# Optimization experiments

Hardware: AMD Instinct MI355X
Metric: run time of the kernel (lower is better)

The kernel has to match this reference:

```python
import jax, jax.numpy as jnp
import numpy as np

HIDDEN = 2048
NUM_HEADS = 32
NUM_GROUPS = 8
HEAD_DIM = HIDDEN // NUM_HEADS          # 64
GROUP_DIM = HEAD_DIM * NUM_GROUPS       # 512
HPG = NUM_HEADS // NUM_GROUPS           # heads per group = 4
B, S = 2, 2048


def setup_inputs() -> dict:
    key = jax.random.key(0)
    ks = jax.random.split(key, 6)
    sd = 1.0 / np.sqrt(HIDDEN)
    return {
        "x": jax.random.normal(ks[0], (B, S, HIDDEN), jnp.float32),
        "mask": jnp.ones((1, 1, S, S), jnp.int32),
        "Wq": jax.random.normal(ks[1], (HIDDEN, HIDDEN), jnp.float32) * sd,
        "bq": jnp.zeros((HIDDEN,), jnp.float32),
        "Wk": jax.random.normal(ks[2], (HIDDEN, GROUP_DIM), jnp.float32) * sd,
        "bk": jnp.zeros((GROUP_DIM,), jnp.float32),
        "Wv": jax.random.normal(ks[3], (HIDDEN, GROUP_DIM), jnp.float32) * sd,
        "bv": jnp.zeros((GROUP_DIM,), jnp.float32),
        "Wo": jax.random.normal(ks[4], (HIDDEN, HIDDEN), jnp.float32) * sd,
        "bo": jnp.zeros((HIDDEN,), jnp.float32),
    }


def reference(x, mask, Wq, bq, Wk, bk, Wv, bv, Wo, bo):
    b, s, _ = x.shape
    # projections
    q = x @ Wq + bq                                        # [B,S,H*d]
    k = x @ Wk + bk                                        # [B,S,G*d]
    v = x @ Wv + bv
    # split heads: q heads are group-major (g, p) to match the torch view
    q = q.reshape(b, s, NUM_GROUPS, HPG, HEAD_DIM)         # [B,S,G,P,d]
    k = k.reshape(b, s, NUM_GROUPS, HEAD_DIM)              # [B,S,G,d]
    v = v.reshape(b, s, NUM_GROUPS, HEAD_DIM)
    scale = 1.0 / np.sqrt(HEAD_DIM).astype(np.float32)
    # grouped attention without materializing repeated K/V
    scores = jnp.einsum('bsgpd,btgd->bgpst', q, k) * scale  # [B,G,P,S,T]
    if mask is not None:
        m = mask[:, :, None]                                # [1,1,1,S,T]
        scores = jnp.where(m == 0, jnp.float32(-1e9), scores)
    weights = jax.nn.softmax(scores, axis=-1)
    out = jnp.einsum('bgpst,btgd->bsgpd', weights, v)       # [B,S,G,P,d]
    out = out.reshape(b, s, HIDDEN)
    return out @ Wo + bo
```

## Files before the change

kernel.cpp:

```cpp
#include <hip/hip_runtime.h>
#include <hip/hip_bf16.h>


#define DEVINL __device__ __forceinline__

typedef __attribute__((ext_vector_type(8))) short bf16x8;
typedef __attribute__((ext_vector_type(4))) float f32x4;

DEVINL unsigned short f2bf(float f) {
  unsigned u = __builtin_bit_cast(unsigned, f);
  u += 0x7fffu + ((u >> 16) & 1u);
  return (unsigned short)(u >> 16);
}

DEVINL unsigned pk2bf(float a, float b) {
  __hip_bfloat162 h = __float22bfloat162_rn(float2{a, b});
  unsigned r;
  __builtin_memcpy(&r, &h, 4);
  return r;
}

DEVINL void gl_lds16(const void* g, void* l) {
  __builtin_amdgcn_global_load_lds(
      (const __attribute__((address_space(1))) void*)g,
      (__attribute__((address_space(3))) void*)l, 16, 0, 0);
}

__global__ __launch_bounds__(256)
void prep_k(const float* __restrict__ x,
            const float* __restrict__ Wq, const float* __restrict__ Wk,
            const float* __restrict__ Wv, const float* __restrict__ Wo,
            const int* __restrict__ mask,
            unsigned short* __restrict__ xb,
            unsigned short* __restrict__ WqT, unsigned short* __restrict__ WkT,
            unsigned short* __restrict__ WvT, unsigned short* __restrict__ WoT,
            int* __restrict__ flags)
{
  __shared__ float tile[64][68];
  __shared__ int fl[4];
  int blk = blockIdx.x;
  const int tid = threadIdx.x;
  if (blk < 4096) {
    size_t base = (size_t)blk * 2048 + tid * 8;
    float4 f0 = *(const float4*)&x[base];
    float4 f1 = *(const float4*)&x[base + 4];
    uint4 o;
    o.x = pk2bf(f0.x, f0.y); o.y = pk2bf(f0.z, f0.w);
    o.z = pk2bf(f1.x, f1.y); o.w = pk2bf(f1.z, f1.w);
    *(uint4*)&xb[base] = o;
    return;
  }
  blk -= 4096;
  if (blk >= 2560) {
    int fb = blk - 2560;
    int qt = fb >> 5, tt = fb & 31;
    bool hz = false;
#pragma unroll
    for (int it = 0; it < 8; ++it) {
      int l = it * 1024 + tid * 4;
      int row = l >> 6, col = l & 63;
      int4 mv = *(const int4*)&mask[(size_t)(qt * 128 + row) * 2048 + tt * 64 + col];
      hz |= (mv.x == 0) | (mv.y == 0) | (mv.z == 0) | (mv.w == 0);
    }
    unsigned long long bal = __ballot(hz);
    if ((tid & 63) == 0) fl[tid >> 6] = (bal != 0ull) ? 1 : 0;
    __syncthreads();
    if (tid == 0) flags[fb] = fl[0] | fl[1] | fl[2] | fl[3];
    return;
  }
  const float* W; unsigned short* WT; int N;
  if (blk < 1024)      { W = Wq; WT = WqT; N = 2048; }
  else if (blk < 1280) { W = Wk; WT = WkT; N = 512;  blk -= 1024; }
  else if (blk < 1536) { W = Wv; WT = WvT; N = 512;  blk -= 1280; }
  else                 { W = Wo; WT = WoT; N = 2048; blk -= 1536; }
  const int kt = blk & 31, nt = blk >> 5;
  const int k0 = kt * 64, n0 = nt * 64;
  const int tr = tid >> 4, tc4 = (tid & 15) * 4;
#pragma unroll
  for (int it = 0; it < 4; ++it) {
    int k = it * 16 + tr;
    float4 v = *(const float4*)&W[(size_t)(k0 + k) * N + n0 + tc4];
    tile[tc4 + 0][k] = v.x; tile[tc4 + 1][k] = v.y;
    tile[tc4 + 2][k] = v.z; tile[tc4 + 3][k] = v.w;
  }
  __syncthreads();
#pragma unroll
  for (int it = 0; it < 4; ++it) {
    int n = it * 16 + tr;
    uint2 o;
    o.x = pk2bf(tile[n][tc4 + 0], tile[n][tc4 + 1]);
    o.y = pk2bf(tile[n][tc4 + 2], tile[n][tc4 + 3]);
    *(uint2*)&WT[(size_t)(n0 + n) * 2048 + k0 + tc4] = o;
  }
}

__global__ __launch_bounds__(256)
void mm_qkv(const unsigned short* __restrict__ A,
            const unsigned short* __restrict__ Wt,
            const float* __restrict__ bq, const float* __restrict__ bk,
            const float* __restrict__ bv,
            unsigned short* __restrict__ qb, unsigned short* __restrict__ kb,
            unsigned short* __restrict__ vb)
{
  __shared__ __align__(16) unsigned short As[128 * 32];
  __shared__ __align__(16) unsigned short Bs[128 * 32];
  const int tid = threadIdx.x;
  const int lane = tid & 63, w = tid >> 6;
  const int l15 = lane & 15, quad = lane >> 4;
  const int wm = w & 1, wn = w >> 1;
  const int row0 = blockIdx.y * 128;
  const int col0 = blockIdx.x * 128;

  f32x4 acc[4][4];
#pragma unroll
  for (int mt = 0; mt < 4; ++mt)
#pragma unroll
    for (int nt = 0; nt < 4; ++nt) acc[mt][nt] = (f32x4){0.f, 0.f, 0.f, 0.f};

  const int c0 = tid, c1 = 256 + tid;
  const size_t aoff0 = (size_t)(row0 + (c0 >> 2)) * 2048 + (c0 & 3) * 8;
  const size_t aoff1 = (size_t)(row0 + (c1 >> 2)) * 2048 + (c1 & 3) * 8;
  const size_t boff0 = (size_t)(col0 + (c0 >> 2)) * 2048 + (c0 & 3) * 8;
  const size_t boff1 = (size_t)(col0 + (c1 >> 2)) * 2048 + (c1 & 3) * 8;

  for (int k0 = 0; k0 < 2048; k0 += 32) {
    gl_lds16(A + aoff0 + k0, As + (size_t)c0 * 8);
    gl_lds16(A + aoff1 + k0, As + (size_t)c1 * 8);
    gl_lds16(Wt + boff0 + k0, Bs + (size_t)c0 * 8);
    gl_lds16(Wt + boff1 + k0, Bs + (size_t)c1 * 8);
    __syncthreads();
    bf16x8 af[4], bfr[4];
#pragma unroll
    for (int mt = 0; mt < 4; ++mt)
      af[mt] = *(const bf16x8*)&As[(wm * 64 + mt * 16 + l15) * 32 + quad * 8];
#pragma unroll
    for (int nt = 0; nt < 4; ++nt)
      bfr[nt] = *(const bf16x8*)&Bs[(wn * 64 + nt * 16 + l15) * 32 + quad * 8];
#pragma unroll
    for (int mt = 0; mt < 4; ++mt)
#pragma unroll
      for (int nt = 0; nt < 4; ++nt)
        acc[mt][nt] = __builtin_amdgcn_mfma_f32_16x16x32_bf16(
            af[mt], bfr[nt], acc[mt][nt], 0, 0, 0);
    __syncthreads();
  }

  const int rbase = row0 + wm * 64 + quad * 4;
#pragma unroll
  for (int nt = 0; nt < 4; ++nt) {
    const int cg = col0 + wn * 64 + nt * 16 + l15;
#pragma unroll
    for (int mt = 0; mt < 4; ++mt) {
#pragma unroll
      for (int reg = 0; reg < 4; ++reg) {
        const int r = rbase + mt * 16 + reg;
        const int bb = r >> 11, ss = r & 2047;
        float v = acc[mt][nt][reg];
        if (col0 < 2048) {
          v += bq[cg];
          int g = cg >> 8, p = (cg >> 6) & 3, d = cg & 63;
          qb[(((size_t)((bb * 8 + g) * 4 + p)) * 2048 + ss) * 64 + d] =
              f2bf(v * 0.1803368801111244f);
        } else if (col0 < 2560) {
          int cl = cg - 2048;
          v += bk[cl];
          int g = cl >> 6, d = cl & 63;
          kb[((size_t)(bb * 8 + g) * 2048 + ss) * 64 + d] = f2bf(v);
        } else {
          int cl = cg - 2560;
          v += bv[cl];
          int g = cl >> 6, d = cl & 63;
          vb[((size_t)(bb * 8 + g) * 64 + d) * 2048 + ss] = f2bf(v);
        }
      }
    }
  }
}

__global__ __launch_bounds__(256)
void mm_out(const unsigned short* __restrict__ A,
            const unsigned short* __restrict__ Bt,
            const float* __restrict__ bias, float* __restrict__ Of)
{
  __shared__ __align__(16) unsigned short As[128 * 32];
  __shared__ __align__(16) unsigned short Bs[128 * 32];
  const int tid = threadIdx.x;
  const int lane = tid & 63, w = tid >> 6;
  const int l15 = lane & 15, quad = lane >> 4;
  const int wm = w & 1, wn = w >> 1;
  const int row0 = blockIdx.y * 128;
  const int col0 = blockIdx.x * 128;

  f32x4 acc[4][4];
#pragma unroll
  for (int mt = 0; mt < 4; ++mt)
#pragma unroll
    for (int nt = 0; nt < 4; ++nt) acc[mt][nt] = (f32x4){0.f, 0.f, 0.f, 0.f};

  const int c0 = tid, c1 = 256 + tid;
  const size_t aoff0 = (size_t)(row0 + (c0 >> 2)) * 2048 + (c0 & 3) * 8;
  const size_t aoff1 = (size_t)(row0 + (c1 >> 2)) * 2048 + (c1 & 3) * 8;
  const size_t boff0 = (size_t)(col0 + (c0 >> 2)) * 2048 + (c0 & 3) * 8;
  const size_t boff1 = (size_t)(col0 + (c1 >> 2)) * 2048 + (c1 & 3) * 8;

  for (int k0 = 0; k0 < 2048; k0 += 32) {
    gl_lds16(A + aoff0 + k0, As + (size_t)c0 * 8);
    gl_lds16(A + aoff1 + k0, As + (size_t)c1 * 8);
    gl_lds16(Bt + boff0 + k0, Bs + (size_t)c0 * 8);
    gl_lds16(Bt + boff1 + k0, Bs + (size_t)c1 * 8);
    __syncthreads();
    bf16x8 af[4], bfr[4];
#pragma unroll
    for (int mt = 0; mt < 4; ++mt)
      af[mt] = *(const bf16x8*)&As[(wm * 64 + mt * 16 + l15) * 32 + quad * 8];
#pragma unroll
    for (int nt = 0; nt < 4; ++nt)
      bfr[nt] = *(const bf16x8*)&Bs[(wn * 64 + nt * 16 + l15) * 32 + quad * 8];
#pragma unroll
    for (int mt = 0; mt < 4; ++mt)
#pragma unroll
      for (int nt = 0; nt < 4; ++nt)
        acc[mt][nt] = __builtin_amdgcn_mfma_f32_16x16x32_bf16(
            af[mt], bfr[nt], acc[mt][nt], 0, 0, 0);
    __syncthreads();
  }

  const int rbase = row0 + wm * 64 + quad * 4;
#pragma unroll
  for (int nt = 0; nt < 4; ++nt) {
    const int cg = col0 + wn * 64 + nt * 16 + l15;
    const float bvv = bias[cg];
#pragma unroll
    for (int mt = 0; mt < 4; ++mt)
#pragma unroll
      for (int reg = 0; reg < 4; ++reg) {
        const int r = rbase + mt * 16 + reg;
        Of[(size_t)r * 2048 + cg] = acc[mt][nt][reg] + bvv;
      }
  }
}

__global__ __launch_bounds__(256, 3)
void attn_k(const unsigned short* __restrict__ qb,
            const unsigned short* __restrict__ kb,
            const unsigned short* __restrict__ vb,
            const int* __restrict__ mask, const int* __restrict__ flags,
            unsigned short* __restrict__ attnb)
{
  __shared__ __align__(16) unsigned short Ks[2][64 * 64];
  __shared__ __align__(16) unsigned short Vs[2][64 * 64];
  __shared__ __align__(16) unsigned short Ps[128 * 72];
  const int tid = threadIdx.x;
  const int lane = tid & 63, w = tid >> 6;
  const int l15 = lane & 15, quad = lane >> 4;
  const int q0 = blockIdx.x * 128;
  const int pr = blockIdx.y;
  const int b = pr >> 5, g = (pr >> 2) & 7, p = pr & 3;
  const int bg = b * 8 + g;

  const unsigned short* Kg = kb + (size_t)bg * 2048 * 64;
  const unsigned short* Vg = vb + (size_t)bg * 64 * 2048;
  const unsigned short* Qg = qb + (size_t)(bg * 4 + p) * 2048 * 64;

  bf16x8 qf[2][2];
#pragma unroll
  for (int u = 0; u < 2; ++u) {
    const size_t qrow = (size_t)(q0 + w * 32 + u * 16 + l15) * 64;
    qf[u][0] = *(const bf16x8*)&Qg[qrow + quad * 8];
    qf[u][1] = *(const bf16x8*)&Qg[qrow + 32 + quad * 8];
  }

  bf16x8 ones;
#pragma unroll
  for (int i = 0; i < 8; ++i) ones[i] = (short)0x3F80;

  f32x4 acc_o[4][2];
  f32x4 acc_l[2];
#pragma unroll
  for (int u = 0; u < 2; ++u) acc_l[u] = (f32x4){0.f, 0.f, 0.f, 0.f};
#pragma unroll
  for (int dt = 0; dt < 4; ++dt)
#pragma unroll
    for (int u = 0; u < 2; ++u) acc_o[dt][u] = (f32x4){0.f, 0.f, 0.f, 0.f};

  const int c0 = tid, c1 = 256 + tid;
  const int kr0 = c0 >> 3, kx0 = ((c0 & 7) ^ (kr0 & 7)) * 8;
  const int kr1 = c1 >> 3, kx1 = ((c1 & 7) ^ (kr1 & 7)) * 8;

  gl_lds16(Kg + (size_t)kr0 * 64 + kx0, &Ks[0][(size_t)c0 * 8]);
  gl_lds16(Kg + (size_t)kr1 * 64 + kx1, &Ks[0][(size_t)c1 * 8]);
  gl_lds16(Vg + (size_t)kr0 * 2048 + kx0, &Vs[0][(size_t)c0 * 8]);
  gl_lds16(Vg + (size_t)kr1 * 2048 + kx1, &Vs[0][(size_t)c1 * 8]);
  __syncthreads();

  for (int it = 0; it < 32; ++it) {
    const int cur = it & 1;
    const int t0 = it << 6;
    if (it < 31) {
      const int tn = t0 + 64;
      gl_lds16(Kg + (size_t)(tn + kr0) * 64 + kx0, &Ks[cur ^ 1][(size_t)c0 * 8]);
      gl_lds16(Kg + (size_t)(tn + kr1) * 64 + kx1, &Ks[cur ^ 1][(size_t)c1 * 8]);
      gl_lds16(Vg + (size_t)kr0 * 2048 + tn + kx0, &Vs[cur ^ 1][(size_t)c0 * 8]);
      gl_lds16(Vg + (size_t)kr1 * 2048 + tn + kx1, &Vs[cur ^ 1][(size_t)c1 * 8]);
    }
    const unsigned short* Kc = Ks[cur];
    const unsigned short* Vc = Vs[cur];

    bf16x8 kf[4][2];
#pragma unroll
    for (int nt = 0; nt < 4; ++nt) {
      const int trow = nt * 16 + l15, ks = trow & 7;
      kf[nt][0] = *(const bf16x8*)&Kc[trow * 64 + ((quad ^ ks) * 8)];
      kf[nt][1] = *(const bf16x8*)&Kc[trow * 64 + (((4 + quad) ^ ks) * 8)];
    }
    const bool msk = flags[blockIdx.x * 32 + it] != 0;

#pragma unroll
    for (int u = 0; u < 2; ++u) {
      f32x4 st[4];
#pragma unroll
      for (int nt = 0; nt < 4; ++nt) {
        f32x4 z = (f32x4){0.f, 0.f, 0.f, 0.f};
        z = __builtin_amdgcn_mfma_f32_16x16x32_bf16(kf[nt][0], qf[u][0], z, 0, 0, 0);
        st[nt] = __builtin_amdgcn_mfma_f32_16x16x32_bf16(kf[nt][1], qf[u][1], z, 0, 0, 0);
      }
      if (msk) {
        const size_t mrow = (size_t)(q0 + w * 32 + u * 16 + l15) * 2048;
#pragma unroll
        for (int nt = 0; nt < 4; ++nt) {
          int4 mv = *(const int4*)&mask[mrow + t0 + nt * 16 + quad * 4];
          if (mv.x == 0) st[nt][0] = -1e30f;
          if (mv.y == 0) st[nt][1] = -1e30f;
          if (mv.z == 0) st[nt][2] = -1e30f;
          if (mv.w == 0) st[nt][3] = -1e30f;
        }
      }
      const int srow = w * 32 + u * 16 + l15;
#pragma unroll
      for (int nt = 0; nt < 4; ++nt) {
        float p0 = __builtin_amdgcn_exp2f(st[nt][0]);
        float p1 = __builtin_amdgcn_exp2f(st[nt][1]);
        float p2 = __builtin_amdgcn_exp2f(st[nt][2]);
        float p3 = __builtin_amdgcn_exp2f(st[nt][3]);
        uint2 pkd;
        pkd.x = pk2bf(p0, p1);
        pkd.y = pk2bf(p2, p3);
        *(uint2*)&Ps[srow * 72 + nt * 16 + quad * 4] = pkd;
      }
    }
    asm volatile("s_waitcnt lgkmcnt(0)" ::: "memory");

    bf16x8 pf[2][2];
#pragma unroll
    for (int u = 0; u < 2; ++u) {
      const int srow = w * 32 + u * 16 + l15;
      pf[u][0] = *(const bf16x8*)&Ps[srow * 72 + quad * 8];
      pf[u][1] = *(const bf16x8*)&Ps[srow * 72 + 32 + quad * 8];
      acc_l[u] = __builtin_amdgcn_mfma_f32_16x16x32_bf16(ones, pf[u][0], acc_l[u], 0, 0, 0);
      acc_l[u] = __builtin_amdgcn_mfma_f32_16x16x32_bf16(ones, pf[u][1], acc_l[u], 0, 0, 0);
    }
#pragma unroll
    for (int dt = 0; dt < 4; ++dt) {
      const int drow = dt * 16 + l15, ks = drow & 7;
      bf16x8 v0 = *(const bf16x8*)&Vc[drow * 64 + ((quad ^ ks) * 8)];
      bf16x8 v1 = *(const bf16x8*)&Vc[drow * 64 + (((4 + quad) ^ ks) * 8)];
#pragma unroll
      for (int u = 0; u < 2; ++u) {
        acc_o[dt][u] = __builtin_amdgcn_mfma_f32_16x16x32_bf16(v0, pf[u][0], acc_o[dt][u], 0, 0, 0);
        acc_o[dt][u] = __builtin_amdgcn_mfma_f32_16x16x32_bf16(v1, pf[u][1], acc_o[dt][u], 0, 0, 0);
      }
    }
    __syncthreads();
  }

  const int hh = g * 4 + p;
#pragma unroll
  for (int u = 0; u < 2; ++u) {
    const float inv = 1.0f / acc_l[u][0];
    const int s = q0 + w * 32 + u * 16 + l15;
#pragma unroll
    for (int dt = 0; dt < 4; ++dt) {
      uint2 o;
      o.x = pk2bf(acc_o[dt][u][0] * inv, acc_o[dt][u][1] * inv);
      o.y = pk2bf(acc_o[dt][u][2] * inv, acc_o[dt][u][3] * inv);
      *(uint2*)&attnb[((size_t)(b * 2048 + s)) * 2048 + hh * 64 + dt * 16 + quad * 4] = o;
    }
  }
}

extern "C" void kernel_launch(void* const* d_in, const int* in_sizes, int n_in,
                              void* d_out, int out_size, void* d_ws, size_t ws_size,
                              hipStream_t stream)
{
  (void)in_sizes; (void)n_in; (void)out_size; (void)ws_size;
  const float* x  = (const float*)d_in[0];
  const int* mask = (const int*)d_in[1];
  const float* Wq = (const float*)d_in[2];
  const float* bq = (const float*)d_in[3];
  const float* Wk = (const float*)d_in[4];
  const float* bk = (const float*)d_in[5];
  const float* Wv = (const float*)d_in[6];
  const float* bv = (const float*)d_in[7];
  const float* Wo = (const float*)d_in[8];
  const float* bo = (const float*)d_in[9];
  float* out = (float*)d_out;

  unsigned short* xb  = (unsigned short*)d_ws;
  unsigned short* WqT = xb  + 8388608;
  unsigned short* WkT = WqT + 4194304;
  unsigned short* WvT = WkT + 1048576;
  unsigned short* WoT = WvT + 1048576;
  unsigned short* qb  = WoT + 4194304;
  unsigned short* kb  = qb  + 8388608;
  unsigned short* vb  = kb  + 2097152;
  int* flags = (int*)(vb + 2097152);
  unsigned short* attnb = xb;

  dim3 blk(256);
  hipLaunchKernelGGL(prep_k, dim3(7168), blk, 0, stream,
                     x, Wq, Wk, Wv, Wo, mask, xb, WqT, WkT, WvT, WoT, flags);
  hipLaunchKernelGGL(mm_qkv, dim3(24, 32), blk, 0, stream,
                     xb, WqT, bq, bk, bv, qb, kb, vb);
  hipLaunchKernelGGL(attn_k, dim3(16, 64), blk, 0, stream,
                     qb, kb, vb, mask, flags, attnb);
  hipLaunchKernelGGL(mm_out, dim3(16, 32), blk, 0, stream,
                     attnb, WoT, bo, out);
}
```

Before: 348.8 us.

## Rework projection GEMMs into 256x256-tile, multi-stage pipelined, swizzled LDS kernels

Both projection GEMMs (QKV and output) now share a macro-based main loop. Each 512-thread block computes a 256x256 tile and streams K in 32-wide halves with global_load_lds. Loads are kept in flight across stages with vmcnt waits and raw barriers instead of a full sync per step, and the LDS layout uses an XOR swizzle to avoid bank conflicts. MFMA sections are wrapped in s_setprio to favour math issue. The larger tiles cut global traffic and synchronisation, but they shrink the grids to 192 and 128 blocks, which may leave many CUs idle, and they use about 128KB of LDS per block.

```diff
diff --git a/kernel.cpp b/kernel.cpp
--- a/kernel.cpp
+++ b/kernel.cpp
@@ -94,7 +94,85 @@
   }
 }
 
-__global__ __launch_bounds__(256)
+
+#define GEMM_WAITB() do { \
+    asm volatile("s_waitcnt vmcnt(8)" ::: "memory"); \
+    __builtin_amdgcn_s_barrier(); \
+  } while (0)
+
+#define GEMM_STAGE(t, kh) do { \
+    const int _b = (t) & 1; \
+    const size_t _ko = (size_t)(t) * 64 + (kh) * 32; \
+    unsigned short* _lA = As + ((_b * 2 + (kh)) * 8192) + tid * 8; \
+    unsigned short* _lB = Bs + ((_b * 2 + (kh)) * 8192) + tid * 8; \
+    gl_lds16(Asrc0 + _ko, _lA); \
+    gl_lds16(Asrc1 + _ko, _lA + 4096); \
+    gl_lds16(Bsrc0 + _ko, _lB); \
+    gl_lds16(Bsrc1 + _ko, _lB + 4096); \
+  } while (0)
+
+#define GEMM_HALFGROUP(t, kh) do { \
+    bf16x8 bfr[4]; \
+    const unsigned short* _base = As + (((t) & 1) * 2 + (kh)) * 8192; \
+    const unsigned short* _bbase = Bs + (((t) & 1) * 2 + (kh)) * 8192; \
+    _Pragma("unroll") \
+    for (int nt = 0; nt < 4; ++nt) { \
+      const int brow = wn * 64 + nt * 16 + l15; \
+      bfr[nt] = *(const bf16x8*)&_bbase[brow * 32 + ((quad ^ ((brow >> 1) & 3)) * 8)]; \
+    } \
+    _Pragma("unroll") \
+    for (int mh = 0; mh < 2; ++mh) { \
+      bf16x8 af[4]; \
+      _Pragma("unroll") \
+      for (int mt = 0; mt < 4; ++mt) { \
+        const int arow = wm * 128 + mh * 64 + mt * 16 + l15; \
+        af[mt] = *(const bf16x8*)&_base[arow * 32 + ((quad ^ ((arow >> 1) & 3)) * 8)]; \
+      } \
+      __builtin_amdgcn_s_setprio(1); \
+      _Pragma("unroll") \
+      for (int mt = 0; mt < 4; ++mt) \
+        _Pragma("unroll") \
+        for (int nt = 0; nt < 4; ++nt) \
+          acc[mh * 4 + mt][nt] = __builtin_amdgcn_mfma_f32_16x16x32_bf16( \
+              af[mt], bfr[nt], acc[mh * 4 + mt][nt], 0, 0, 0); \
+      __builtin_amdgcn_s_setprio(0); \
+    } \
+  } while (0)
+
+#define GEMM_KLOOP_BODY(Aptr, Bptr) \
+  const int tid = threadIdx.x; \
+  const int lane = tid & 63, l15 = lane & 15, quad = lane >> 4; \
+  const int w = tid >> 6, wm = w & 1, wn = w >> 1; \
+  const int row0 = blockIdx.y * 256; \
+  const int col0 = blockIdx.x * 256; \
+  f32x4 acc[8][4]; \
+  _Pragma("unroll") \
+  for (int am = 0; am < 8; ++am) \
+    _Pragma("unroll") \
+    for (int nt = 0; nt < 4; ++nt) acc[am][nt] = (f32x4){0.f, 0.f, 0.f, 0.f}; \
+  const int e0 = tid, e1 = tid + 512; \
+  const int sr0 = e0 >> 2, sc0 = ((e0 & 3) ^ ((sr0 >> 1) & 3)) * 8; \
+  const int sr1 = e1 >> 2, sc1 = ((e1 & 3) ^ ((sr1 >> 1) & 3)) * 8; \
+  const unsigned short* Asrc0 = (Aptr) + (size_t)(row0 + sr0) * 2048 + sc0; \
+  const unsigned short* Asrc1 = (Aptr) + (size_t)(row0 + sr1) * 2048 + sc1; \
+  const unsigned short* Bsrc0 = (Bptr) + (size_t)(col0 + sr0) * 2048 + sc0; \
+  const unsigned short* Bsrc1 = (Bptr) + (size_t)(col0 + sr1) * 2048 + sc1; \
+  GEMM_STAGE(0, 0); \
+  GEMM_STAGE(0, 1); \
+  GEMM_STAGE(1, 0); \
+  GEMM_WAITB(); \
+  for (int t = 0; t < 32; ++t) { \
+    const int tn1 = (t + 1 < 32) ? t + 1 : 31; \
+    const int tn2 = (t + 2 < 32) ? t + 2 : 31; \
+    GEMM_STAGE(tn1, 1); \
+    GEMM_HALFGROUP(t, 0); \
+    GEMM_WAITB(); \
+    GEMM_STAGE(tn2, 0); \
+    GEMM_HALFGROUP(t, 1); \
+    GEMM_WAITB(); \
+  }
+
+__global__ __launch_bounds__(512, 2)
 void mm_qkv(const unsigned short* __restrict__ A,
             const unsigned short* __restrict__ Wt,
             const float* __restrict__ bq, const float* __restrict__ bk,
@@ -102,60 +180,21 @@
             unsigned short* __restrict__ qb, unsigned short* __restrict__ kb,
             unsigned short* __restrict__ vb)
 {
-  __shared__ __align__(16) unsigned short As[128 * 32];
-  __shared__ __align__(16) unsigned short Bs[128 * 32];
-  const int tid = threadIdx.x;
-  const int lane = tid & 63, w = tid >> 6;
-  const int l15 = lane & 15, quad = lane >> 4;
-  const int wm = w & 1, wn = w >> 1;
-  const int row0 = blockIdx.y * 128;
-  const int col0 = blockIdx.x * 128;
-
-  f32x4 acc[4][4];
-#pragma unroll
-  for (int mt = 0; mt < 4; ++mt)
-#pragma unroll
-    for (int nt = 0; nt < 4; ++nt) acc[mt][nt] = (f32x4){0.f, 0.f, 0.f, 0.f};
-
-  const int c0 = tid, c1 = 256 + tid;
-  const size_t aoff0 = (size_t)(row0 + (c0 >> 2)) * 2048 + (c0 & 3) * 8;
-  const size_t aoff1 = (size_t)(row0 + (c1 >> 2)) * 2048 + (c1 & 3) * 8;
-  const size_t boff0 = (size_t)(col0 + (c0 >> 2)) * 2048 + (c0 & 3) * 8;
-  const size_t boff1 = (size_t)(col0 + (c1 >> 2)) * 2048 + (c1 & 3) * 8;
-
-  for (int k0 = 0; k0 < 2048; k0 += 32) {
-    gl_lds16(A + aoff0 + k0, As + (size_t)c0 * 8);
-    gl_lds16(A + aoff1 + k0, As + (size_t)c1 * 8);
-    gl_lds16(Wt + boff0 + k0, Bs + (size_t)c0 * 8);
-    gl_lds16(Wt + boff1 + k0, Bs + (size_t)c1 * 8);
-    __syncthreads();
-    bf16x8 af[4], bfr[4];
-#pragma unroll
-    for (int mt = 0; mt < 4; ++mt)
-      af[mt] = *(const bf16x8*)&As[(wm * 64 + mt * 16 + l15) * 32 + quad * 8];
-#pragma unroll
-    for (int nt = 0; nt < 4; ++nt)
-      bfr[nt] = *(const bf16x8*)&Bs[(wn * 64 + nt * 16 + l15) * 32 + quad * 8];
-#pragma unroll
-    for (int mt = 0; mt < 4; ++mt)
-#pragma unroll
-      for (int nt = 0; nt < 4; ++nt)
-        acc[mt][nt] = __builtin_amdgcn_mfma_f32_16x16x32_bf16(
-            af[mt], bfr[nt], acc[mt][nt], 0, 0, 0);
-    __syncthreads();
-  }
-
-  const int rbase = row0 + wm * 64 + quad * 4;
+  __shared__ __align__(16) unsigned short As[32768];
+  __shared__ __align__(16) unsigned short Bs[32768];
+  GEMM_KLOOP_BODY(A, Wt)
+
+  const int rb = row0 + wm * 128 + quad * 4;
 #pragma unroll
   for (int nt = 0; nt < 4; ++nt) {
     const int cg = col0 + wn * 64 + nt * 16 + l15;
 #pragma unroll
-    for (int mt = 0; mt < 4; ++mt) {
+    for (int am = 0; am < 8; ++am) {
 #pragma unroll
       for (int reg = 0; reg < 4; ++reg) {
-        const int r = rbase + mt * 16 + reg;
+        const int r = rb + am * 16 + reg;
         const int bb = r >> 11, ss = r & 2047;
-        float v = acc[mt][nt][reg];
+        float v = acc[am][nt][reg];
         if (col0 < 2048) {
           v += bq[cg];
           int g = cg >> 8, p = (cg >> 6) & 3, d = cg & 63;
@@ -177,66 +216,28 @@
   }
 }
 
-__global__ __launch_bounds__(256)
+__global__ __launch_bounds__(512, 2)
 void mm_out(const unsigned short* __restrict__ A,
             const unsigned short* __restrict__ Bt,
             const float* __restrict__ bias, float* __restrict__ Of)
 {
-  __shared__ __align__(16) unsigned short As[128 * 32];
-  __shared__ __align__(16) unsigned short Bs[128 * 32];
-  const int tid = threadIdx.x;
-  const int lane = tid & 63, w = tid >> 6;
-  const int l15 = lane & 15, quad = lane >> 4;
-  const int wm = w & 1, wn = w >> 1;
-  const int row0 = blockIdx.y * 128;
-  const int col0 = blockIdx.x * 128;
-
-  f32x4 acc[4][4];
-#pragma unroll
-  for (int mt = 0; mt < 4; ++mt)
-#pragma unroll
-    for (int nt = 0; nt < 4; ++nt) acc[mt][nt] = (f32x4){0.f, 0.f, 0.f, 0.f};
-
-  const int c0 = tid, c1 = 256 + tid;
-  const size_t aoff0 = (size_t)(row0 + (c0 >> 2)) * 2048 + (c0 & 3) * 8;
-  const size_t aoff1 = (size_t)(row0 + (c1 >> 2)) * 2048 + (c1 & 3) * 8;
-  const size_t boff0 = (size_t)(col0 + (c0 >> 2)) * 2048 + (c0 & 3) * 8;
-  const size_t boff1 = (size_t)(col0 + (c1 >> 2)) * 2048 + (c1 & 3) * 8;
-
-  for (int k0 = 0; k0 < 2048; k0 += 32) {
-    gl_lds16(A + aoff0 + k0, As + (size_t)c0 * 8);
-    gl_lds16(A + aoff1 + k0, As + (size_t)c1 * 8);
-    gl_lds16(Bt + boff0 + k0, Bs + (size_t)c0 * 8);
-    gl_lds16(Bt + boff1 + k0, Bs + (size_t)c1 * 8);
-    __syncthreads();
-    bf16x8 af[4], bfr[4];
-#pragma unroll
-    for (int mt = 0; mt < 4; ++mt)
-      af[mt] = *(const bf16x8*)&As[(wm * 64 + mt * 16 + l15) * 32 + quad * 8];
-#pragma unroll
-    for (int nt = 0; nt < 4; ++nt)
-      bfr[nt] = *(const bf16x8*)&Bs[(wn * 64 + nt * 16 + l15) * 32 + quad * 8];
-#pragma unroll
-    for (int mt = 0; mt < 4; ++mt)
-#pragma unroll
-      for (int nt = 0; nt < 4; ++nt)
-        acc[mt][nt] = __builtin_amdgcn_mfma_f32_16x16x32_bf16(
-            af[mt], bfr[nt], acc[mt][nt], 0, 0, 0);
-    __syncthreads();
-  }
-
-  const int rbase = row0 + wm * 64 + quad * 4;
+  __shared__ __align__(16) unsigned short As[32768];
+  __shared__ __align__(16) unsigned short Bs[32768];
+  GEMM_KLOOP_BODY(A, Bt)
+
+  const int rb = row0 + wm * 128 + quad * 4;
 #pragma unroll
   for (int nt = 0; nt < 4; ++nt) {
     const int cg = col0 + wn * 64 + nt * 16 + l15;
     const float bvv = bias[cg];
 #pragma unroll
-    for (int mt = 0; mt < 4; ++mt)
+    for (int am = 0; am < 8; ++am) {
 #pragma unroll
       for (int reg = 0; reg < 4; ++reg) {
-        const int r = rbase + mt * 16 + reg;
-        Of[(size_t)r * 2048 + cg] = acc[mt][nt][reg] + bvv;
-      }
+        const int r = rb + am * 16 + reg;
+        Of[(size_t)r * 2048 + cg] = acc[am][nt][reg] + bvv;
+      }
+    }
   }
 }
 
@@ -416,13 +417,12 @@
   int* flags = (int*)(vb + 2097152);
   unsigned short* attnb = xb;
 
-  dim3 blk(256);
-  hipLaunchKernelGGL(prep_k, dim3(7168), blk, 0, stream,
+  hipLaunchKernelGGL(prep_k, dim3(7168), dim3(256), 0, stream,
                      x, Wq, Wk, Wv, Wo, mask, xb, WqT, WkT, WvT, WoT, flags);
-  hipLaunchKernelGGL(mm_qkv, dim3(24, 32), blk, 0, stream,
+  hipLaunchKernelGGL(mm_qkv, dim3(12, 16), dim3(512), 0, stream,
                      xb, WqT, bq, bk, bv, qb, kb, vb);
-  hipLaunchKernelGGL(attn_k, dim3(16, 64), blk, 0, stream,
+  hipLaunchKernelGGL(attn_k, dim3(16, 64), dim3(256), 0, stream,
                      qb, kb, vb, mask, flags, attnb);
-  hipLaunchKernelGGL(mm_out, dim3(16, 32), blk, 0, stream,
+  hipLaunchKernelGGL(mm_out, dim3(8, 16), dim3(512), 0, stream,
                      attnb, WoT, bo, out);
 }
```

Measured after the change: 383.6 us. 10.0% more time.

## Double attention block to 512 threads and 256 query rows, remap block order

Applied to the files above, without the earlier changes.

The attention kernel now runs 8 waves per block covering 256 query rows, so each K/V tile staged in LDS is shared by twice as many waves, and each thread issues one async global-to-LDS load per K and V tile instead of two. Blocks are remapped so that consecutive block ids fall on different (batch, group, head) pairs. The mask-flag lookup is adjusted to the new query tiling. In exchange the grid halves, the P buffer doubles in LDS, and launch bounds change to 512 threads with a minimum of 4 blocks, which may tighten per-thread register limits and spill.

```diff
diff --git a/kernel.cpp b/kernel.cpp
--- a/kernel.cpp
+++ b/kernel.cpp
@@ -240,7 +240,7 @@
   }
 }
 
-__global__ __launch_bounds__(256, 3)
+__global__ __launch_bounds__(512, 4)
 void attn_k(const unsigned short* __restrict__ qb,
             const unsigned short* __restrict__ kb,
             const unsigned short* __restrict__ vb,
@@ -249,12 +249,16 @@
 {
   __shared__ __align__(16) unsigned short Ks[2][64 * 64];
   __shared__ __align__(16) unsigned short Vs[2][64 * 64];
-  __shared__ __align__(16) unsigned short Ps[128 * 72];
+  __shared__ __align__(16) unsigned short Ps[256 * 72];
   const int tid = threadIdx.x;
   const int lane = tid & 63, w = tid >> 6;
   const int l15 = lane & 15, quad = lane >> 4;
-  const int q0 = blockIdx.x * 128;
-  const int pr = blockIdx.y;
+
+  const int lid = blockIdx.y * 8 + blockIdx.x;
+  const int work = (lid & 7) * 64 + (lid >> 3);
+  const int qt = work & 7;
+  const int pr = work >> 3;
+  const int q0 = qt * 256;
   const int b = pr >> 5, g = (pr >> 2) & 7, p = pr & 3;
   const int bg = b * 8 + g;
 
@@ -283,14 +287,11 @@
 #pragma unroll
     for (int u = 0; u < 2; ++u) acc_o[dt][u] = (f32x4){0.f, 0.f, 0.f, 0.f};
 
-  const int c0 = tid, c1 = 256 + tid;
-  const int kr0 = c0 >> 3, kx0 = ((c0 & 7) ^ (kr0 & 7)) * 8;
-  const int kr1 = c1 >> 3, kx1 = ((c1 & 7) ^ (kr1 & 7)) * 8;
-
-  gl_lds16(Kg + (size_t)kr0 * 64 + kx0, &Ks[0][(size_t)c0 * 8]);
-  gl_lds16(Kg + (size_t)kr1 * 64 + kx1, &Ks[0][(size_t)c1 * 8]);
-  gl_lds16(Vg + (size_t)kr0 * 2048 + kx0, &Vs[0][(size_t)c0 * 8]);
-  gl_lds16(Vg + (size_t)kr1 * 2048 + kx1, &Vs[0][(size_t)c1 * 8]);
+  const int kr = tid >> 3;
+  const int kx = ((tid & 7) ^ (kr & 7)) * 8;
+
+  gl_lds16(Kg + (size_t)kr * 64 + kx, &Ks[0][(size_t)tid * 8]);
+  gl_lds16(Vg + (size_t)kr * 2048 + kx, &Vs[0][(size_t)tid * 8]);
   __syncthreads();
 
   for (int it = 0; it < 32; ++it) {
@@ -298,10 +299,8 @@
     const int t0 = it << 6;
     if (it < 31) {
       const int tn = t0 + 64;
-      gl_lds16(Kg + (size_t)(tn + kr0) * 64 + kx0, &Ks[cur ^ 1][(size_t)c0 * 8]);
-      gl_lds16(Kg + (size_t)(tn + kr1) * 64 + kx1, &Ks[cur ^ 1][(size_t)c1 * 8]);
-      gl_lds16(Vg + (size_t)kr0 * 2048 + tn + kx0, &Vs[cur ^ 1][(size_t)c0 * 8]);
-      gl_lds16(Vg + (size_t)kr1 * 2048 + tn + kx1, &Vs[cur ^ 1][(size_t)c1 * 8]);
+      gl_lds16(Kg + (size_t)(tn + kr) * 64 + kx, &Ks[cur ^ 1][(size_t)tid * 8]);
+      gl_lds16(Vg + (size_t)kr * 2048 + tn + kx, &Vs[cur ^ 1][(size_t)tid * 8]);
     }
     const unsigned short* Kc = Ks[cur];
     const unsigned short* Vc = Vs[cur];
@@ -313,7 +312,7 @@
       kf[nt][0] = *(const bf16x8*)&Kc[trow * 64 + ((quad ^ ks) * 8)];
       kf[nt][1] = *(const bf16x8*)&Kc[trow * 64 + (((4 + quad) ^ ks) * 8)];
     }
-    const bool msk = flags[blockIdx.x * 32 + it] != 0;
+    const bool msk = flags[(qt * 2 + (w >> 2)) * 32 + it] != 0;
 
 #pragma unroll
     for (int u = 0; u < 2; ++u) {
@@ -416,13 +415,12 @@
   int* flags = (int*)(vb + 2097152);
   unsigned short* attnb = xb;
 
-  dim3 blk(256);
-  hipLaunchKernelGGL(prep_k, dim3(7168), blk, 0, stream,
+  hipLaunchKernelGGL(prep_k, dim3(7168), dim3(256), 0, stream,
                      x, Wq, Wk, Wv, Wo, mask, xb, WqT, WkT, WvT, WoT, flags);
-  hipLaunchKernelGGL(mm_qkv, dim3(24, 32), blk, 0, stream,
+  hipLaunchKernelGGL(mm_qkv, dim3(24, 32), dim3(256), 0, stream,
                      xb, WqT, bq, bk, bv, qb, kb, vb);
-  hipLaunchKernelGGL(attn_k, dim3(16, 64), blk, 0, stream,
+  hipLaunchKernelGGL(attn_k, dim3(8, 64), dim3(512), 0, stream,
                      qb, kb, vb, mask, flags, attnb);
-  hipLaunchKernelGGL(mm_out, dim3(16, 32), blk, 0, stream,
+  hipLaunchKernelGGL(mm_out, dim3(16, 32), dim3(256), 0, stream,
                      attnb, WoT, bo, out);
 }
```

After: 349.2 us. About the same (+0.1%).
